# Performance work log

Hardware: AMD Instinct MI355X
Metric: run time of the kernel (lower is better)

## Reference

```python
import jax, jax.numpy as jnp
import numpy as np

B, L, D, H, HD, K = 1, 1024, 1024, 16, 64, 16
EPS = 1e-5

def _l2norm(x):
    n = jnp.sqrt(jnp.sum(x * x, axis=-1, keepdims=True))
    return x / jnp.maximum(n, 1e-12)

def _lin(x, w, b):
    return x @ w.T + b

def _lrelu2(x, alpha=0.01):
    y = jnp.where(x > 0, x, alpha * x)
    return y * y

def _forward(x, spectral_basis, M_phi_w, M_phi_b, wq_w, wq_b, wk_w, wk_b,
             wv_w, wv_b, wo_w, wo_b, wg_z_w, wg_z_b, kv_norm_scale):
    Bx, Lx, Dx = x.shape
    bhld = x.reshape(Bx, Lx, H, HD).transpose(0, 2, 1, 3)          # [B,H,L,h]
    # stu_conv: causal conv of every channel with each of K shared filters (FFT form)
    n = 2 * Lx
    Xf = jnp.fft.rfft(bhld, n=n, axis=2)                            # [B,H,F,h]
    Ff = jnp.fft.rfft(spectral_basis, n=n, axis=0)                  # [F,K]
    conv = jnp.fft.irfft(Xf[:, :, :, None, :] * Ff[None, None, :, :, None], n=n, axis=2)[:, :, :Lx]  # [B,H,L,K,h]
    x_tilde = conv.transpose(0, 2, 3, 1, 4).reshape(Bx, Lx, K * H * HD)
    x_tilde = _lin(x_tilde, M_phi_w, M_phi_b)                       # [B,L,D]
    q = _lin(x_tilde, wq_w, wq_b).reshape(Bx, Lx, H, HD).transpose(0, 2, 1, 3)
    k = _lin(x_tilde, wk_w, wk_b).reshape(Bx, Lx, H, HD).transpose(0, 2, 1, 3)
    v = _lin(x_tilde, wv_w, wv_b).reshape(Bx, Lx, H, HD).transpose(0, 2, 1, 3)
    k = _l2norm(k)
    v = _l2norm(v)
    sim = jnp.einsum('bhld,bhld->bhl', q, k)                        # [B,H,L]
    # Z[b,h,s,p,n] = k[b,h,s,n] * v[b,h,s,p]
    Z = v[..., :, None] * k[..., None, :]                           # [B,H,L,h,h]
    Z = Z * kv_norm_scale
    gates_logits = Z.reshape(Bx, H, Lx, HD * HD) @ wg_z_w.T + wg_z_b  # [B,H,L,1]
    gates_z = (_lrelu2(gates_logits) + EPS)[..., 0]                 # [B,H,L]
    gated_Z = Z * gates_z[..., None, None]
    # online-softmax associative scan over sequence: running (max, norm, exp-weighted v)
    def combine(a, b):
        ma, na, va = a
        mb, nb, vb = b
        m = jnp.maximum(ma, mb)
        ea = jnp.exp(ma - m)
        eb = jnp.exp(mb - m)
        return (m, na * ea + nb * eb, va * ea[..., None] + vb * eb[..., None])
    max_cumul, norm_cumul, v_cumul = jax.lax.associative_scan(
        combine, (sim, jnp.ones_like(sim), v), axis=2)
    Z_cumul = jnp.cumsum(gated_Z, axis=2)
    gate_cumul = jnp.cumsum(gates_z, axis=2)
    linear_attn = v_cumul / (norm_cumul[..., None] + EPS)           # [B,H,L,h]
    weights = jnp.exp(sim - max_cumul) / (norm_cumul + EPS)         # [B,H,L]
    Hm = Z_cumul / (gate_cumul[..., None, None] + EPS)              # [B,H,L,h,h]
    Y_base = jnp.einsum('bhtp,bhtpn->bhtn', q, Hm)                  # [B,H,L,h]
    # torch einsum broadcasts the size-1 p-dim of linear_attn.unsqueeze(-2):
    Y_lin = jnp.sum(q, axis=-1, keepdims=True) * linear_attn        # [B,H,L,h]
    Y = Y_base + (Y_lin - Y_base) * weights[..., None]
    Y = Y.transpose(0, 2, 1, 3).reshape(Bx, Lx, Dx)
    Y = _l2norm(Y)
    return _lin(Y, wo_w, wo_b)

def setup_inputs() -> dict:
    key = jax.random.key(0)
    ks = jax.random.split(key, 16)
    def nrm(k, shape, scale):
        return jax.random.normal(k, shape, dtype=jnp.float32) * scale
    return {
        'x': nrm(ks[0], (B, L, D), 1.0),
        'spectral_basis': nrm(ks[1], (L, K), 1.0 / np.sqrt(L)),
        'M_phi_w': nrm(ks[2], (D, K * H * HD), 1.0 / np.sqrt(K * H * HD)),
        'M_phi_b': jnp.zeros((D,), jnp.float32),
        'wq_w': nrm(ks[3], (D, D), 1.0 / np.sqrt(D)),
        'wq_b': jnp.zeros((D,), jnp.float32),
        'wk_w': nrm(ks[4], (D, D), 1.0 / np.sqrt(D)),
        'wk_b': jnp.zeros((D,), jnp.float32),
        'wv_w': nrm(ks[5], (D, D), 1.0 / np.sqrt(D)),
        'wv_b': jnp.zeros((D,), jnp.float32),
        'wo_w': nrm(ks[6], (D, D), 1.0 / np.sqrt(D)),
        'wo_b': jnp.zeros((D,), jnp.float32),
        'wg_z_w': nrm(ks[7], (1, HD * HD), 1.0 / np.sqrt(HD * HD)),
        'wg_z_b': jnp.zeros((1,), jnp.float32),
        'kv_norm_scale': jnp.ones((1, H, 1, 1, 1), jnp.float32),
    }

def reference(x, spectral_basis, M_phi_w, M_phi_b, wq_w, wq_b, wk_w, wk_b,
              wv_w, wv_b, wo_w, wo_b, wg_z_w, wg_z_b, kv_norm_scale):
    return _forward(x, spectral_basis, M_phi_w, M_phi_b, wq_w, wq_b, wk_w, wk_b,
                    wv_w, wv_b, wo_w, wo_b, wg_z_w, wg_z_b, kv_norm_scale)
```

## Files before the change

kernel.cpp:

```cpp
#include <hip/hip_runtime.h>
#include <hip/hip_bf16.h>

typedef __hip_bfloat16 bf16;
typedef __attribute__((ext_vector_type(8))) short short8;
typedef __attribute__((ext_vector_type(4))) float f32x4;

struct bf16x8 { bf16 v[8]; };
struct bf16x4 { bf16 v[4]; };

__device__ __forceinline__ void gload_lds16(const void* g, void* l) {
  __builtin_amdgcn_global_load_lds(
      (const __attribute__((address_space(1))) void*)g,
      (__attribute__((address_space(3))) void*)l, 16, 0, 0);
}

__device__ __forceinline__ float wave_sum(float x) {
#pragma unroll
  for (int o = 32; o > 0; o >>= 1) x += __shfl_xor(x, o, 64);
  return x;
}

__global__ void prep_cast_k(const float* __restrict__ mphiW,
                            const float* __restrict__ wq, const float* __restrict__ wk,
                            const float* __restrict__ wv, const float* __restrict__ wo,
                            const float* __restrict__ x,
                            const float* __restrict__ bq, const float* __restrict__ bk,
                            const float* __restrict__ bv,
                            bf16* __restrict__ mphi_bf, bf16* __restrict__ wqkv,
                            bf16* __restrict__ wo_bf, bf16* __restrict__ x_bf,
                            float* __restrict__ qkv_bias) {
  int b = blockIdx.x, tid = threadIdx.x;
  const float* src; bf16* dst; int i;
  if (b < 8192) { src = mphiW; dst = mphi_bf; i = b * 256 + tid; }
  else if (b < 10240) {
    int bb = b - 8192;
    src = (bb < 512) ? wq : (bb < 1024) ? wk : (bb < 1536) ? wv : wo;
    dst = (bb < 512) ? wqkv : (bb < 1024) ? (wqkv + 1048576)
         : (bb < 1536) ? (wqkv + 2097152) : wo_bf;
    i = (bb & 511) * 256 + tid;
  } else if (b < 10752) { src = x; dst = x_bf; i = (b - 10240) * 256 + tid; }
  else {
    int j = (b - 10752) * 256 + tid;
    if (j < 3072) {
      const float* s = (j < 1024) ? bq : (j < 2048) ? bk : bv;
      qkv_bias[j] = s[j & 1023];
    }
    return;
  }
  const float4* p = (const float4*)src + (size_t)i * 2;
  float4 a = p[0], c = p[1];
  bf16x8 o;
  o.v[0] = __float2bfloat16(a.x); o.v[1] = __float2bfloat16(a.y);
  o.v[2] = __float2bfloat16(a.z); o.v[3] = __float2bfloat16(a.w);
  o.v[4] = __float2bfloat16(c.x); o.v[5] = __float2bfloat16(c.y);
  o.v[6] = __float2bfloat16(c.z); o.v[7] = __float2bfloat16(c.w);
  ((bf16x8*)dst)[i] = o;
}

__global__ void build_T_k(const float* __restrict__ basis, bf16* __restrict__ T) {
  size_t i8 = (size_t)blockIdx.x * 256 + threadIdx.x;
  size_t i = i8 * 8;
  int s0 = (int)(i & 1023);
  int l = (int)((i >> 10) & 1023);
  int k = (int)(i >> 20);
  bf16x8 o;
#pragma unroll
  for (int j = 0; j < 8; j++) {
    int s = s0 + j;
    o.v[j] = (s <= l) ? __float2bfloat16(basis[(size_t)(l - s) * 16 + k])
                      : __float2bfloat16(0.f);
  }
  ((bf16x8*)T)[i8] = o;
}

template<int TRI, int OUTBF, int HASB, int DBUF>
__global__ void gemm_bt(const bf16* __restrict__ A, long sAb, int lda,
                        const bf16* __restrict__ B, long sBb, int ldb,
                        void* __restrict__ Cv, void* __restrict__ Cv2, int nbz1,
                        long sCb, int ldc,
                        const float* __restrict__ bias, int sbias, int K) {
  constexpr int NB = DBUF ? 2 : 1;
  __shared__ bf16 As[NB][128 * 64];
  __shared__ bf16 Bs[NB][128 * 64];
  const int tid = threadIdx.x;
  const int lane = tid & 63;
  const int wid = tid >> 6;
  const int wr = wid >> 1, wc = wid & 1;
  const int cpx = gridDim.x >> 3;
  const int logical = (blockIdx.x & 7) * cpx + (blockIdx.x >> 3);
  const int bx = logical & 7, by = (logical >> 3) & 7, bz = logical >> 6;
  const int r0 = by * 128, c0 = bx * 128;
  const bf16* Ab = A + (size_t)bz * sAb;
  const bf16* Bb = B + (size_t)bz * sBb;
  f32x4 acc[4][4] = {};
  const int nt = (TRI ? min(K, r0 + 128) : K) >> 6;

  const int srow = tid >> 3, scol = (tid & 7) << 3;

#define STAGE(buf, t)                                                         \
  {                                                                           \
    const int k0_ = (t) << 6;                                                 \
    _Pragma("unroll")                                                         \
    for (int i = 0; i < 4; i++) {                                             \
      int row = i * 32 + srow;                                                \
      gload_lds16(Ab + (size_t)(r0 + row) * lda + k0_ + scol,                 \
                  &As[buf][(row << 6) + scol]);                               \
    }                                                                         \
    _Pragma("unroll")                                                         \
    for (int i = 0; i < 4; i++) {                                             \
      int row = i * 32 + srow;                                                \
      gload_lds16(Bb + (size_t)(c0 + row) * ldb + k0_ + scol,                 \
                  &Bs[buf][(row << 6) + scol]);                               \
    }                                                                         \
  }

  int cur = 0;
  if (DBUF) STAGE(0, 0)
  for (int t = 0; t < nt; ++t) {
    if (DBUF) {
      if (t + 1 < nt) {
        STAGE(cur ^ 1, t + 1)
        asm volatile("s_waitcnt vmcnt(8)" ::: "memory");
      } else {
        asm volatile("s_waitcnt vmcnt(0)" ::: "memory");
      }
      __syncthreads();
    } else {
      __syncthreads();
      STAGE(0, t)
      asm volatile("s_waitcnt vmcnt(0)" ::: "memory");
      __syncthreads();
    }
#pragma unroll
    for (int ks = 0; ks < 2; ks++) {
      const int colo = ks * 32 + (lane >> 4) * 8;
      short8 af[4], bfr[4];
#pragma unroll
      for (int m = 0; m < 4; m++)
        af[m] = *(const short8*)&As[cur][(wr * 64 + m * 16 + (lane & 15)) * 64 + colo];
#pragma unroll
      for (int n = 0; n < 4; n++)
        bfr[n] = *(const short8*)&Bs[cur][(wc * 64 + n * 16 + (lane & 15)) * 64 + colo];
#pragma unroll
      for (int m = 0; m < 4; m++)
#pragma unroll
        for (int n = 0; n < 4; n++)
          acc[m][n] = __builtin_amdgcn_mfma_f32_16x16x32_bf16(af[m], bfr[n], acc[m][n], 0, 0, 0);
    }
    if (DBUF) { __syncthreads(); cur ^= 1; }
  }
#undef STAGE

  void* Cb = (bz < nbz1) ? Cv : Cv2;
  const int bzl = (bz < nbz1) ? bz : bz - nbz1;
  const int rb = r0 + wr * 64 + ((lane >> 4) << 2);
  const int cb = c0 + wc * 64 + (lane & 15);
#pragma unroll
  for (int n = 0; n < 4; n++) {
    const int col = cb + n * 16;
    float bv = HASB ? bias[bz * sbias + col] : 0.f;
#pragma unroll
    for (int m = 0; m < 4; m++) {
#pragma unroll
      for (int j = 0; j < 4; j++) {
        const int row = rb + m * 16 + j;
        size_t off = (size_t)bzl * sCb + (size_t)row * ldc + col;
        float v = acc[m][n][j] + bv;
        if (OUTBF) ((bf16*)Cb)[off] = __float2bfloat16(v);
        else       ((float*)Cb)[off] = v;
      }
    }
  }
}

__global__ void reduce16_k(const float* __restrict__ pA, const float* __restrict__ pB,
                           const float* __restrict__ bias, bf16* __restrict__ out) {
  int i4 = blockIdx.x * 256 + threadIdx.x;
  float4 v = *((const float4*)bias + (i4 & 255));
#pragma unroll
  for (int j = 0; j < 8; j++) {
    float4 a = *((const float4*)pA + i4 + j * 262144);
    v.x += a.x; v.y += a.y; v.z += a.z; v.w += a.w;
  }
#pragma unroll
  for (int j = 0; j < 8; j++) {
    float4 a = *((const float4*)pB + i4 + j * 262144);
    v.x += a.x; v.y += a.y; v.z += a.z; v.w += a.w;
  }
  bf16x4 o;
  o.v[0] = __float2bfloat16(v.x); o.v[1] = __float2bfloat16(v.y);
  o.v[2] = __float2bfloat16(v.z); o.v[3] = __float2bfloat16(v.w);
  ((bf16x4*)out)[i4] = o;
}

__global__ void reduce4f_k(const float* __restrict__ p, const float* __restrict__ bias,
                           float* __restrict__ out) {
  int i4 = blockIdx.x * 256 + threadIdx.x;
  float4 v = *((const float4*)bias + (i4 & 255));
#pragma unroll
  for (int j = 0; j < 4; j++) {
    float4 a = *((const float4*)p + i4 + j * 262144);
    v.x += a.x; v.y += a.y; v.z += a.z; v.w += a.w;
  }
  ((float4*)out)[i4] = v;
}

__global__ void qkv_post_k(const float* __restrict__ qkv, const float* __restrict__ W,
                           const float* __restrict__ wgb, const float* __restrict__ scale,
                           float* __restrict__ kn, float* __restrict__ vn,
                           float* __restrict__ sim, float* __restrict__ gz, float* __restrict__ qs) {
  __shared__ float Wl[64][65];
  int tid = threadIdx.x;
#pragma unroll
  for (int i = 0; i < 16; i++) {
    int c = i * 256 + tid;
    Wl[c >> 6][c & 63] = W[c];
  }
  __syncthreads();
  int lane = tid & 63;
  int gw = blockIdx.x * 4 + (tid >> 6);
  int h = gw >> 10, l = gw & 1023;
  const float* base = qkv + (size_t)l * 1024 + h * 64 + lane;
  float q = base[0];
  float k = base[1048576];
  float v = base[2097152];
  float knv = k * (1.f / fmaxf(sqrtf(wave_sum(k * k)), 1e-12f));
  float vnv = v * (1.f / fmaxf(sqrtf(wave_sum(v * v)), 1e-12f));
  float simv = wave_sum(q * knv);
  float qsv = wave_sum(q);
  float inner = 0.f;
#pragma unroll 8
  for (int n = 0; n < 64; n++)
    inner += Wl[lane][n] * __shfl(knv, n, 64);
  float gl = wave_sum(vnv * inner) * scale[h] + wgb[0];
  float yy = gl > 0.f ? gl : 0.01f * gl;
  float gzz = yy * yy + 1e-5f;
  size_t o = ((size_t)h * 1024 + l) * 64 + lane;
  kn[o] = knv; vn[o] = vnv;
  if (lane == 0) {
    sim[h * 1024 + l] = simv; gz[h * 1024 + l] = gzz; qs[h * 1024 + l] = qsv;
  }
}

__global__ void scan_outer_k(const float* __restrict__ sim, const float* __restrict__ gz,
                             const float* __restrict__ vn, const float* __restrict__ kn,
                             float* __restrict__ vloc, float* __restrict__ mloc,
                             float* __restrict__ nloc, float* __restrict__ gloc,
                             float* __restrict__ mA, float* __restrict__ nA,
                             float* __restrict__ vA, float* __restrict__ gA,
                             float* __restrict__ Mc) {
  __shared__ float vns[64][64], kns[64][64], gzs[64];
  int c = blockIdx.x, h = blockIdx.y, tid = threadIdx.x;
  size_t base = ((size_t)h * 1024 + c * 64) * 64;
#pragma unroll
  for (int i = 0; i < 16; i++) {
    int e = i * 256 + tid;
    vns[e >> 6][e & 63] = vn[base + e];
    kns[e >> 6][e & 63] = kn[base + e];
  }
  if (tid < 64) gzs[tid] = gz[h * 1024 + c * 64 + tid];
  __syncthreads();
  float acc[16] = {};
  for (int s = 0; s < 64; s++) {
    float g = gzs[s];
#pragma unroll
    for (int i = 0; i < 16; i++) {
      int pn = i * 256 + tid;
      acc[i] += (g * vns[s][pn >> 6]) * kns[s][pn & 63];
    }
  }
  size_t ob = (size_t)(h * 16 + c) * 4096;
#pragma unroll
  for (int i = 0; i < 16; i++) Mc[ob + i * 256 + tid] = acc[i];
  if (tid < 64) {
    int lane = tid;
    size_t hb = (size_t)h * 1024 + c * 64;
    float m = -1e30f, n = 0.f, v = 0.f, g = 0.f;
    for (int i = 0; i < 64; i++) {
      float s = sim[hb + i];
      float vv = vns[i][lane];
      float mn = fmaxf(m, s);
      float eo = expf(m - mn);
      float en = expf(s - mn);
      n = n * eo + en;
      v = v * eo + en * vv;
      m = mn;
      g += gzs[i];
      vloc[(hb + i) * 64 + lane] = v;
      if (lane == 0) { mloc[hb + i] = m; nloc[hb + i] = n; gloc[hb + i] = g; }
    }
    size_t ix = (size_t)h * 16 + c;
    vA[ix * 64 + lane] = v;
    if (lane == 0) { mA[ix] = m; nA[ix] = n; gA[ix] = g; }
  }
}

__launch_bounds__(256)
__global__ void apply_attn_k(const float* __restrict__ qkvf, const float* __restrict__ vn,
                             const float* __restrict__ kn, const float* __restrict__ gz,
                             const float* __restrict__ sim, const float* __restrict__ qs,
                             const float* __restrict__ mloc, const float* __restrict__ nloc,
                             const float* __restrict__ gloc, const float* __restrict__ vloc,
                             const float* __restrict__ mA, const float* __restrict__ nA,
                             const float* __restrict__ gA, const float* __restrict__ vA,
                             const float* __restrict__ Mc, const float* __restrict__ scale,
                             float* __restrict__ linb, float* __restrict__ Yc) {
  __shared__ float qls[64][65], vls[64][65], kls[64][68];
  __shared__ float SP[4096];
  __shared__ float gzs[64], wt_s[64], gc_s[64];
  float (*P)[33] = (float(*)[33])SP;
  int c = blockIdx.x, h = blockIdx.y, tid = threadIdx.x;
  size_t base = ((size_t)h * 1024 + c * 64) * 64;
#pragma unroll
  for (int i = 0; i < 16; i++) {
    int e = i * 256 + tid;
    int r = e >> 6, cc = e & 63;
    qls[r][cc] = qkvf[(size_t)(c * 64 + r) * 1024 + h * 64 + cc];
    vls[r][cc] = vn[base + e];
    kls[r][cc] = kn[base + e];
  }
  if (tid < 64) gzs[tid] = gz[h * 1024 + c * 64 + tid];
  {
    float4 a0 = {0,0,0,0}, a1 = {0,0,0,0}, a2 = {0,0,0,0}, a3 = {0,0,0,0};
    const float* McH = Mc + (size_t)h * 16 * 4096;
    for (int cc = 0; cc < c; cc++) {
      const float4* p = (const float4*)(McH + cc * 4096) + tid * 4;
      float4 t0v = p[0], t1v = p[1], t2v = p[2], t3v = p[3];
      a0.x += t0v.x; a0.y += t0v.y; a0.z += t0v.z; a0.w += t0v.w;
      a1.x += t1v.x; a1.y += t1v.y; a1.z += t1v.z; a1.w += t1v.w;
      a2.x += t2v.x; a2.y += t2v.y; a2.z += t2v.z; a2.w += t2v.w;
      a3.x += t3v.x; a3.y += t3v.y; a3.z += t3v.z; a3.w += t3v.w;
    }
    float4* Sp = (float4*)SP + tid * 4;
    Sp[0] = a0; Sp[1] = a1; Sp[2] = a2; Sp[3] = a3;
  }
  {
    int lane = tid & 63, w = tid >> 6;
    float m = -1e30f, n = 0.f, v = 0.f, g = 0.f;
    for (int cc = 0; cc < c; cc++) {
      size_t ix = (size_t)h * 16 + cc;
      float mb = mA[ix], nb = nA[ix], gb = gA[ix];
      float vb = vA[ix * 64 + lane];
      float mn = fmaxf(m, mb);
      float ea = expf(m - mn), eb = expf(mb - mn);
      n = n * ea + nb * eb;
      v = v * ea + vb * eb;
      m = mn; g += gb;
    }
#pragma unroll 4
    for (int i = 0; i < 16; i++) {
      int row = w * 16 + i;
      int gw = h * 1024 + c * 64 + row;
      float ml = mloc[gw], nl = nloc[gw], gl = gloc[gw];
      float vl = vloc[(size_t)gw * 64 + lane];
      float mf = fmaxf(m, ml);
      float ep = expf(m - mf), el = expf(ml - mf);
      float nf = n * ep + nl * el;
      float vf = v * ep + vl * el;
      float inv = 1.f / (nf + 1e-5f);
      linb[(size_t)gw * 64 + lane] = vf * inv;
      if (lane == 0) {
        wt_s[row] = expf(sim[gw] - mf) * inv;
        gc_s[row] = g + gl;
      }
    }
  }
  __syncthreads();
  const int t0 = (tid >> 4) * 4, n0 = (tid & 15) * 4;
  float y[4][4] = {};
  for (int p = 0; p < 64; p++) {
    float av[4];
#pragma unroll
    for (int i2 = 0; i2 < 4; i2++) av[i2] = qls[t0 + i2][p];
    float4 bv = *(const float4*)&SP[p * 64 + n0];
#pragma unroll
    for (int i2 = 0; i2 < 4; i2++) {
      y[i2][0] += av[i2] * bv.x; y[i2][1] += av[i2] * bv.y;
      y[i2][2] += av[i2] * bv.z; y[i2][3] += av[i2] * bv.w;
    }
  }
  __syncthreads();
  const int tg = tid >> 3;
  const int s2b = (tid & 7) * 4;
  for (int s0 = 0; s0 < 64; s0 += 32) {
    float pv[2][4] = {};
    for (int k2 = 0; k2 < 64; k2++) {
      float a0 = qls[tg * 2][k2], a1 = qls[tg * 2 + 1][k2];
#pragma unroll
      for (int j = 0; j < 4; j++) {
        float b = vls[s0 + s2b + j][k2];
        pv[0][j] += a0 * b;
        pv[1][j] += a1 * b;
      }
    }
#pragma unroll
    for (int ii = 0; ii < 2; ii++)
#pragma unroll
      for (int j = 0; j < 4; j++) {
        int t = tg * 2 + ii, ss = s0 + s2b + j;
        P[t][ss - s0] = (ss <= t) ? pv[ii][j] * gzs[ss] : 0.f;
      }
    __syncthreads();
    for (int ss = 0; ss < 32; ss++) {
      float pr[4];
#pragma unroll
      for (int i2 = 0; i2 < 4; i2++) pr[i2] = P[t0 + i2][ss];
      float4 kvv = *(const float4*)&kls[s0 + ss][n0];
#pragma unroll
      for (int i2 = 0; i2 < 4; i2++) {
        y[i2][0] += pr[i2] * kvv.x; y[i2][1] += pr[i2] * kvv.y;
        y[i2][2] += pr[i2] * kvv.z; y[i2][3] += pr[i2] * kvv.w;
      }
    }
    __syncthreads();
  }
  float sc = scale[h];
#pragma unroll
  for (int i2 = 0; i2 < 4; i2++) {
    int lrow = t0 + i2;
    int l = c * 64 + lrow;
    size_t il = (size_t)h * 1024 + l;
    float gcv = gc_s[lrow], wv = wt_s[lrow], qv = qs[il];
    float den = 1.f / (gcv + 1e-5f);
    float4 lv = *(const float4*)&linb[il * 64 + n0];
    float yl0 = qv * lv.x, yl1 = qv * lv.y, yl2 = qv * lv.z, yl3 = qv * lv.w;
    float yb0 = sc * y[i2][0] * den, yb1 = sc * y[i2][1] * den;
    float yb2 = sc * y[i2][2] * den, yb3 = sc * y[i2][3] * den;
    float* dst = Yc + (size_t)l * 1024 + h * 64 + n0;
    dst[0] = yb0 + (yl0 - yb0) * wv;
    dst[1] = yb1 + (yl1 - yb1) * wv;
    dst[2] = yb2 + (yl2 - yb2) * wv;
    dst[3] = yb3 + (yl3 - yb3) * wv;
  }
}

__global__ void rownorm_cast_k(const float* __restrict__ Y, bf16* __restrict__ out) {
  __shared__ float red[4];
  int l = blockIdx.x, tid = threadIdx.x;
  float4 v = ((const float4*)(Y + (size_t)l * 1024))[tid];
  float ss = v.x * v.x + v.y * v.y + v.z * v.z + v.w * v.w;
  ss = wave_sum(ss);
  int wid = tid >> 6, lane = tid & 63;
  if (lane == 0) red[wid] = ss;
  __syncthreads();
  float tot = red[0] + red[1] + red[2] + red[3];
  float inv = 1.f / fmaxf(sqrtf(tot), 1e-12f);
  bf16x4 o;
  o.v[0] = __float2bfloat16(v.x * inv); o.v[1] = __float2bfloat16(v.y * inv);
  o.v[2] = __float2bfloat16(v.z * inv); o.v[3] = __float2bfloat16(v.w * inv);
  ((bf16x4*)(out + (size_t)l * 1024))[tid] = o;
}

extern "C" void kernel_launch(void* const* d_in, const int* in_sizes, int n_in,
                              void* d_out, int out_size, void* d_ws, size_t ws_size,
                              hipStream_t stream) {
  (void)in_sizes; (void)n_in; (void)out_size; (void)ws_size;
  const float* x     = (const float*)d_in[0];
  const float* basis = (const float*)d_in[1];
  const float* mphiW = (const float*)d_in[2];
  const float* mphiB = (const float*)d_in[3];
  const float* wqW = (const float*)d_in[4];  const float* wqB = (const float*)d_in[5];
  const float* wkW = (const float*)d_in[6];  const float* wkB = (const float*)d_in[7];
  const float* wvW = (const float*)d_in[8];  const float* wvB = (const float*)d_in[9];
  const float* woW = (const float*)d_in[10]; const float* woB = (const float*)d_in[11];
  const float* wgW = (const float*)d_in[12]; const float* wgB = (const float*)d_in[13];
  const float* kvs = (const float*)d_in[14];
  float* out = (float*)d_out;
  char* ws = (char*)d_ws;

  bf16*  Y_T     = (bf16*)(ws + 0x0000000UL);
  bf16*  Tbuf    = (bf16*)(ws + 0x2000000UL);
  bf16*  mphi_bf = (bf16*)(ws + 0x4000000UL);
  float* part2a  = (float*)(ws + 0x4000000UL);
  float* qkvf    = (float*)(ws + 0x4000000UL);
  float* part8   = (float*)(ws + 0x4000000UL);
  bf16*  x_bf    = (bf16*)(ws + 0x6000000UL);
  bf16*  xtil_bf = (bf16*)(ws + 0x6200000UL);
  bf16*  wqkv_bf = (bf16*)(ws + 0x6400000UL);
  bf16*  wo_bf   = (bf16*)(ws + 0x6A00000UL);
  float* qkv_bias= (float*)(ws + 0x6C00000UL);
  float* part2b  = (float*)(ws + 0x6C10000UL);
  float* kn      = (float*)(ws + 0x6C10000UL);
  float* vn      = (float*)(ws + 0x7010000UL);
  float* Mc      = (float*)(ws + 0x7410000UL);
  float* Yc      = (float*)(ws + 0x7810000UL);
  bf16*  ynorm   = (bf16*)(ws + 0x7C10000UL);
  float* simb    = (float*)(ws + 0x7E10000UL);
  float* gzb     = (float*)(ws + 0x7E20000UL);
  float* qsb     = (float*)(ws + 0x7E30000UL);
  float* vloc = (float*)(ws + 0x2000000UL);
  float* mloc = (float*)(ws + 0x2400000UL);
  float* nloc = (float*)(ws + 0x2410000UL);
  float* gloc = (float*)(ws + 0x2420000UL);
  float* mA   = (float*)(ws + 0x2430000UL);
  float* nA   = (float*)(ws + 0x2431000UL);
  float* gA   = (float*)(ws + 0x2432000UL);
  float* vA   = (float*)(ws + 0x2440000UL);
  float* linb = (float*)(ws + 0x2500000UL);

  prep_cast_k<<<10764, 256, 0, stream>>>(mphiW, wqW, wkW, wvW, woW, x, wqB, wkB, wvB,
                                         mphi_bf, wqkv_bf, wo_bf, x_bf, qkv_bias);
  build_T_k<<<8192, 256, 0, stream>>>(basis, Tbuf);

  gemm_bt<0, 1, 0, 0><<<1024, 256, 0, stream>>>(
      mphi_bf, 1024L, 16384, x_bf, 0L, 1024, (void*)Y_T, (void*)Y_T, 1 << 28,
      1048576L, 1024, nullptr, 0, 1024);

  gemm_bt<1, 0, 0, 0><<<1024, 256, 0, stream>>>(
      Tbuf, 1048576L, 1024, Y_T, 1048576L, 1024, (void*)part2a, (void*)part2b, 8,
      1048576L, 1024, nullptr, 0, 1024);
  reduce16_k<<<1024, 256, 0, stream>>>(part2a, part2b, mphiB, xtil_bf);

  gemm_bt<0, 0, 1, 1><<<192, 256, 0, stream>>>(
      xtil_bf, 0L, 1024, wqkv_bf, 1048576L, 1024, (void*)qkvf, (void*)qkvf, 1 << 28,
      1048576L, 1024, qkv_bias, 1024, 1024);

  qkv_post_k<<<4096, 256, 0, stream>>>(qkvf, wgW, wgB, kvs, kn, vn, simb, gzb, qsb);

  scan_outer_k<<<dim3(16, 16), 256, 0, stream>>>(simb, gzb, vn, kn,
                                                 vloc, mloc, nloc, gloc,
                                                 mA, nA, vA, gA, Mc);

  apply_attn_k<<<dim3(16, 16), 256, 0, stream>>>(qkvf, vn, kn, gzb, simb, qsb,
                                                 mloc, nloc, gloc, vloc,
                                                 mA, nA, gA, vA, Mc, kvs, linb, Yc);

  rownorm_cast_k<<<1024, 256, 0, stream>>>(Yc, ynorm);

  gemm_bt<0, 0, 0, 1><<<256, 256, 0, stream>>>(
      ynorm, 256L, 1024, wo_bf, 256L, 1024, (void*)part8, (void*)part8, 1 << 28,
      1048576L, 1024, nullptr, 0, 256);
  reduce4f_k<<<1024, 256, 0, stream>>>(part8, woB, out);
}
```

Before: 270.5 us.

## Split attention apply into chunk-prefix, scan-apply and matmul kernels

The monolithic apply kernel had each block serially sum all preceding chunk states (up to 15×4096 floats) and run the cross-chunk softmax scan before its matmuls. A new kernel now computes an exclusive prefix of the chunk states once, and a separate kernel does the scan combine, writing the linear output, weights and gate sums to global buffers. The matmul kernel then just loads its precomputed prefix and reads those buffers, with launch bounds asking for two blocks per SM. This removes redundant quadratic prefix work and load imbalance across chunks, at the cost of two extra launches and extra global round trips.

```diff
diff --git a/kernel.cpp b/kernel.cpp
--- a/kernel.cpp
+++ b/kernel.cpp
@@ -295,19 +295,65 @@
   }
 }
 
-__launch_bounds__(256)
-__global__ void apply_attn_k(const float* __restrict__ qkvf, const float* __restrict__ vn,
-                             const float* __restrict__ kn, const float* __restrict__ gz,
-                             const float* __restrict__ sim, const float* __restrict__ qs,
+__global__ void chunk_prefix_k(const float* __restrict__ Mc, float* __restrict__ Sb) {
+  int idx = blockIdx.x * 256 + threadIdx.x;
+  int h = idx >> 12, pn = idx & 4095;
+  float a = 0.f;
+  for (int c = 0; c < 16; c++) {
+    size_t o = (size_t)(h * 16 + c) * 4096 + pn;
+    Sb[o] = a; a += Mc[o];
+  }
+}
+
+__global__ void scan_apply_k(const float* __restrict__ sim,
                              const float* __restrict__ mloc, const float* __restrict__ nloc,
                              const float* __restrict__ gloc, const float* __restrict__ vloc,
                              const float* __restrict__ mA, const float* __restrict__ nA,
                              const float* __restrict__ gA, const float* __restrict__ vA,
-                             const float* __restrict__ Mc, const float* __restrict__ scale,
-                             float* __restrict__ linb, float* __restrict__ Yc) {
+                             float* __restrict__ linb, float* __restrict__ wtb,
+                             float* __restrict__ gcb) {
+  int c = blockIdx.x, h = blockIdx.y;
+  int tid = threadIdx.x, lane = tid & 63, w = tid >> 6;
+  float m = -1e30f, n = 0.f, v = 0.f, g = 0.f;
+  for (int cc = 0; cc < c; cc++) {
+    size_t ix = (size_t)h * 16 + cc;
+    float mb = mA[ix], nb = nA[ix], gb = gA[ix];
+    float vb = vA[ix * 64 + lane];
+    float mn = fmaxf(m, mb);
+    float ea = expf(m - mn), eb = expf(mb - mn);
+    n = n * ea + nb * eb;
+    v = v * ea + vb * eb;
+    m = mn; g += gb;
+  }
+#pragma unroll 4
+  for (int i = 0; i < 16; i++) {
+    int row = w * 16 + i;
+    int gw = h * 1024 + c * 64 + row;
+    float ml = mloc[gw], nl = nloc[gw], gl = gloc[gw];
+    float vl = vloc[(size_t)gw * 64 + lane];
+    float mf = fmaxf(m, ml);
+    float ep = expf(m - mf), el = expf(ml - mf);
+    float nf = n * ep + nl * el;
+    float vf = v * ep + vl * el;
+    float inv = 1.f / (nf + 1e-5f);
+    linb[(size_t)gw * 64 + lane] = vf * inv;
+    if (lane == 0) {
+      wtb[gw] = expf(sim[gw] - mf) * inv;
+      gcb[gw] = g + gl;
+    }
+  }
+}
+
+__launch_bounds__(256, 2)
+__global__ void attn_mm_k(const float* __restrict__ qkvf, const float* __restrict__ vn,
+                          const float* __restrict__ kn, const float* __restrict__ gz,
+                          const float* __restrict__ qs, const float* __restrict__ Sb,
+                          const float* __restrict__ wtb, const float* __restrict__ gcb,
+                          const float* __restrict__ linb, const float* __restrict__ scale,
+                          float* __restrict__ Yc) {
   __shared__ float qls[64][65], vls[64][65], kls[64][68];
   __shared__ float SP[4096];
-  __shared__ float gzs[64], wt_s[64], gc_s[64];
+  __shared__ float gzs[64];
   float (*P)[33] = (float(*)[33])SP;
   int c = blockIdx.x, h = blockIdx.y, tid = threadIdx.x;
   size_t base = ((size_t)h * 1024 + c * 64) * 64;
@@ -321,49 +367,10 @@
   }
   if (tid < 64) gzs[tid] = gz[h * 1024 + c * 64 + tid];
   {
-    float4 a0 = {0,0,0,0}, a1 = {0,0,0,0}, a2 = {0,0,0,0}, a3 = {0,0,0,0};
-    const float* McH = Mc + (size_t)h * 16 * 4096;
-    for (int cc = 0; cc < c; cc++) {
-      const float4* p = (const float4*)(McH + cc * 4096) + tid * 4;
-      float4 t0v = p[0], t1v = p[1], t2v = p[2], t3v = p[3];
-      a0.x += t0v.x; a0.y += t0v.y; a0.z += t0v.z; a0.w += t0v.w;
-      a1.x += t1v.x; a1.y += t1v.y; a1.z += t1v.z; a1.w += t1v.w;
-      a2.x += t2v.x; a2.y += t2v.y; a2.z += t2v.z; a2.w += t2v.w;
-      a3.x += t3v.x; a3.y += t3v.y; a3.z += t3v.z; a3.w += t3v.w;
-    }
-    float4* Sp = (float4*)SP + tid * 4;
-    Sp[0] = a0; Sp[1] = a1; Sp[2] = a2; Sp[3] = a3;
-  }
-  {
-    int lane = tid & 63, w = tid >> 6;
-    float m = -1e30f, n = 0.f, v = 0.f, g = 0.f;
-    for (int cc = 0; cc < c; cc++) {
-      size_t ix = (size_t)h * 16 + cc;
-      float mb = mA[ix], nb = nA[ix], gb = gA[ix];
-      float vb = vA[ix * 64 + lane];
-      float mn = fmaxf(m, mb);
-      float ea = expf(m - mn), eb = expf(mb - mn);
-      n = n * ea + nb * eb;
-      v = v * ea + vb * eb;
-      m = mn; g += gb;
-    }
-#pragma unroll 4
-    for (int i = 0; i < 16; i++) {
-      int row = w * 16 + i;
-      int gw = h * 1024 + c * 64 + row;
-      float ml = mloc[gw], nl = nloc[gw], gl = gloc[gw];
-      float vl = vloc[(size_t)gw * 64 + lane];
-      float mf = fmaxf(m, ml);
-      float ep = expf(m - mf), el = expf(ml - mf);
-      float nf = n * ep + nl * el;
-      float vf = v * ep + vl * el;
-      float inv = 1.f / (nf + 1e-5f);
-      linb[(size_t)gw * 64 + lane] = vf * inv;
-      if (lane == 0) {
-        wt_s[row] = expf(sim[gw] - mf) * inv;
-        gc_s[row] = g + gl;
-      }
-    }
+    const float4* Sg = (const float4*)(Sb + ((size_t)h * 16 + c) * 4096);
+    float4* Sp = (float4*)SP;
+#pragma unroll
+    for (int j = 0; j < 4; j++) Sp[tid * 4 + j] = Sg[tid * 4 + j];
   }
   __syncthreads();
   const int t0 = (tid >> 4) * 4, n0 = (tid & 15) * 4;
@@ -420,7 +427,7 @@
     int lrow = t0 + i2;
     int l = c * 64 + lrow;
     size_t il = (size_t)h * 1024 + l;
-    float gcv = gc_s[lrow], wv = wt_s[lrow], qv = qs[il];
+    float gcv = gcb[il], wv = wtb[il], qv = qs[il];
     float den = 1.f / (gcv + 1e-5f);
     float4 lv = *(const float4*)&linb[il * 64 + n0];
     float yl0 = qv * lv.x, yl1 = qv * lv.y, yl2 = qv * lv.z, yl3 = qv * lv.w;
@@ -488,6 +495,8 @@
   float* simb    = (float*)(ws + 0x7E10000UL);
   float* gzb     = (float*)(ws + 0x7E20000UL);
   float* qsb     = (float*)(ws + 0x7E30000UL);
+  float* wtb     = (float*)(ws + 0x7E40000UL);
+  float* gcb     = (float*)(ws + 0x7E50000UL);
   float* vloc = (float*)(ws + 0x2000000UL);
   float* mloc = (float*)(ws + 0x2400000UL);
   float* nloc = (float*)(ws + 0x2410000UL);
@@ -497,6 +506,7 @@
   float* gA   = (float*)(ws + 0x2432000UL);
   float* vA   = (float*)(ws + 0x2440000UL);
   float* linb = (float*)(ws + 0x2500000UL);
+  float* Sb   = (float*)(ws + 0x2900000UL);
 
   prep_cast_k<<<10764, 256, 0, stream>>>(mphiW, wqW, wkW, wvW, woW, x, wqB, wkB, wvB,
                                          mphi_bf, wqkv_bf, wo_bf, x_bf, qkv_bias);
@@ -521,9 +531,12 @@
                                                  vloc, mloc, nloc, gloc,
                                                  mA, nA, vA, gA, Mc);
 
-  apply_attn_k<<<dim3(16, 16), 256, 0, stream>>>(qkvf, vn, kn, gzb, simb, qsb,
-                                                 mloc, nloc, gloc, vloc,
-                                                 mA, nA, gA, vA, Mc, kvs, linb, Yc);
+  chunk_prefix_k<<<256, 256, 0, stream>>>(Mc, Sb);
+  scan_apply_k<<<dim3(16, 16), 256, 0, stream>>>(simb, mloc, nloc, gloc, vloc,
+                                                 mA, nA, gA, vA, linb, wtb, gcb);
+
+  attn_mm_k<<<dim3(16, 16), 256, 0, stream>>>(qkvf, vn, kn, gzb, qsb, Sb,
+                                              wtb, gcb, linb, kvs, Yc);
 
   rownorm_cast_k<<<1024, 256, 0, stream>>>(Yc, ynorm);
 
```

Measured after the change: 357.4 us. 1.32x slower.
